# Kernel optimization log

Hardware: AMD Instinct MI355X
Metric: run time of the kernel (lower is better)

The kernel has to match this reference:

```python
import jax, jax.numpy as jnp
import numpy as np

ENTRY_SIZE = 8192
TUPLE_SIZE = 16
N_NEURONS = ENTRY_SIZE // TUPLE_SIZE            # 512
ADDR_SPACE = 2 ** TUPLE_SIZE                     # 65536
BATCH = 4096


def setup_inputs() -> dict:
    key = jax.random.key(0)
    k1, k2, k3 = jax.random.split(key, 3)
    # Binary input bits [B, entry_size]
    inp = jax.random.randint(k1, (BATCH, ENTRY_SIZE), 0, 2, dtype=jnp.int32)
    # Permutation mapping bits -> tuples (identity permutation; arange fill)
    tuple_mapping = jnp.arange(ENTRY_SIZE, dtype=jnp.int64)
    # Dense RAM tables emulating the per-neuron dicts:
    #   counts[n, a] = number of training samples that hit address a in neuron n
    #                  (0 means the address was never trained -> not in dict)
    #   sums[n, a]   = accumulated target sum for that address
    counts = jax.random.randint(k2, (N_NEURONS, ADDR_SPACE), 0, 4, dtype=jnp.int32)
    sums = jax.random.normal(k3, (N_NEURONS, ADDR_SPACE), dtype=jnp.float32)
    return {"input": inp, "tuple_mapping": tuple_mapping, "counts": counts, "sums": sums}


def reference(input, tuple_mapping, counts, sums):
    """RegressionWisard.predict with centrality='mean'.

    input:  [B, entry_size] binary bits (int32)
    tuple_mapping: [entry_size] permutation (int)
    counts: [n_neurons, 2^tuple_size] int32 RAM hit counts
    sums:   [n_neurons, 2^tuple_size] float32 RAM target sums
    """
    B = input.shape[0]
    # Map and group bits into tuples: [B, N, T]
    mapped = jnp.take(input, tuple_mapping, axis=1).reshape(B, N_NEURONS, TUPLE_SIZE)
    # Binary address per (sample, neuron); tidx flips so bit 0 is the MSB.
    pow2 = (jnp.int32(1) << jnp.arange(TUPLE_SIZE - 1, -1, -1, dtype=jnp.int32))
    addr = jnp.einsum("bnt,t->bn", mapped, pow2)  # [B, N], values in [0, 2^T)
    neuron_idx = jnp.arange(N_NEURONS, dtype=jnp.int32)[None, :]  # [1, N]
    c = counts[neuron_idx, addr]  # [B, N]
    s = sums[neuron_idx, addr]    # [B, N]
    trained = c > 0               # dict-membership (torch.isin) equivalent
    response = jnp.sum(jnp.where(trained, s, jnp.float32(0)), axis=1)      # [B]
    counters = jnp.sum(jnp.where(trained, c, 0), axis=1).astype(s.dtype)   # [B]
    return jnp.nan_to_num(response / counters)
```

## Files before the change

kernel.cpp:

```cpp
#include <hip/hip_runtime.h>


typedef float f32x4 __attribute__((ext_vector_type(4)));
typedef int   i32x4 __attribute__((ext_vector_type(4)));

constexpr int BATCH   = 4096;
constexpr int ENTRY   = 8192;
constexpr int TUP     = 16;
constexpr int NEUR    = ENTRY / TUP;
constexpr int SPB_A   = 4;
constexpr int QSPLIT  = 8;
constexpr int QSIZE   = 65536 / QSPLIT;

constexpr size_t ADDR_BYTES = (size_t)NEUR * BATCH * 2;
constexpr size_t ACC_OFF    = ADDR_BYTES;
constexpr size_t WS_NEED    = ADDR_BYTES + (size_t)BATCH * 8;

__global__ __launch_bounds__(256) void zero_acc_kernel(unsigned long long* acc) {
    acc[blockIdx.x * 256 + threadIdx.x] = 0ull;
}

__global__ __launch_bounds__(256) void phaseA_kernel(
    const int* __restrict__ input,
    const int* __restrict__ mapping,
    unsigned short* __restrict__ addr_out)
{
    __shared__ unsigned int packed[SPB_A][ENTRY / 32];
    const int tid  = threadIdx.x;
    const int lane = tid & 63;
    const int wv   = tid >> 6;
    const int b0   = blockIdx.x * SPB_A;
    constexpr int CH = ENTRY / 64;

    for (int i0 = wv * 4; i0 < SPB_A * CH; i0 += 16) {
        int v[4];
        #pragma unroll
        for (int u = 0; u < 4; ++u) {
            const int i = i0 + u, r = i >> 7, c = i & 127;
            v[u] = __builtin_nontemporal_load(
                &input[(size_t)(b0 + r) * ENTRY + c * 64 + lane]);
        }
        #pragma unroll
        for (int u = 0; u < 4; ++u) {
            const int i = i0 + u, r = i >> 7, c = i & 127;
            const unsigned long long m = __ballot(v[u] & 1);
            if (lane == 0) {
                packed[r][c * 2]     = (unsigned int)(m);
                packed[r][c * 2 + 1] = (unsigned int)(m >> 32);
            }
        }
    }
    __syncthreads();

    #pragma unroll
    for (int k = 0; k < 2; ++k) {
        const int n = tid + k * 256;
        const int* map_n = mapping + n * TUP;
        int addr[SPB_A] = {0, 0, 0, 0};
        #pragma unroll
        for (int t = 0; t < TUP; ++t) {
            const int j = map_n[t];
            const unsigned w = j >> 5, sh = j & 31;
            #pragma unroll
            for (int s = 0; s < SPB_A; ++s)
                addr[s] = (addr[s] << 1) | ((packed[s][w] >> sh) & 1);
        }
        uint2 pk;
        pk.x = (unsigned)addr[0] | ((unsigned)addr[1] << 16);
        pk.y = (unsigned)addr[2] | ((unsigned)addr[3] << 16);
        *(uint2*)(addr_out + (size_t)n * BATCH + b0) = pk;
    }
}

__global__ __launch_bounds__(256) void phaseB_kernel(
    const int*   __restrict__ counts,
    const float* __restrict__ sums,
    const unsigned short* __restrict__ addr,
    unsigned long long* __restrict__ acc)
{
    __shared__ float         s_tab[QSIZE];
    __shared__ unsigned char c_tab[QSIZE];
    const int tid = threadIdx.x;
    const int n   = blockIdx.x >> 3;
    const int q   = blockIdx.x & (QSPLIT - 1);
    const size_t base = ((size_t)n << 16) + ((size_t)q * QSIZE);

    const f32x4* s4 = (const f32x4*)(sums + base);
    const i32x4* c4 = (const i32x4*)(counts + base);
    f32x4 vs[8]; i32x4 vc[8];
    #pragma unroll
    for (int i = 0; i < 8; ++i) vs[i] = __builtin_nontemporal_load(&s4[tid + 256 * i]);
    #pragma unroll
    for (int i = 0; i < 8; ++i) vc[i] = __builtin_nontemporal_load(&c4[tid + 256 * i]);
    #pragma unroll
    for (int i = 0; i < 8; ++i) {
        ((f32x4*)s_tab)[tid + 256 * i] = vs[i];
        *(uchar4*)&c_tab[(tid + 256 * i) * 4] =
            make_uchar4((unsigned char)vc[i].x, (unsigned char)vc[i].y,
                        (unsigned char)vc[i].z, (unsigned char)vc[i].w);
    }
    __syncthreads();

    const unsigned short* arow = addr + ((size_t)n << 12);
    #pragma unroll
    for (int i = tid; i < BATCH; i += 256) {
        const int a = arow[i];
        if ((a >> 13) == q) {
            const int local = a & (QSIZE - 1);
            const int c = c_tab[local];
            if (c) {
                const long long r = (long long)__float2int_rn(s_tab[local] * 16777216.0f);
                atomicAdd(&acc[i], (unsigned long long)((r << 20) + (long long)c));
            }
        }
    }
}

__global__ __launch_bounds__(256) void phaseC_kernel(
    const unsigned long long* __restrict__ acc, float* __restrict__ out)
{
    const int i = blockIdx.x * 256 + threadIdx.x;
    const long long v = (long long)acc[i];
    const int cnt = (int)(v & 0xFFFFF);
    const long long rq = v >> 20;
    out[i] = (cnt > 0)
        ? (float)(((double)rq * (1.0 / 16777216.0)) / (double)cnt)
        : 0.0f;
}

__global__ __launch_bounds__(256) void wisard_direct_kernel(
    const int* __restrict__ input, const int* __restrict__ mapping,
    const int* __restrict__ counts, const float* __restrict__ sums,
    float* __restrict__ out)
{
    __shared__ unsigned int packed[ENTRY / 32];
    __shared__ float s_resp[4];
    __shared__ int   s_cnt [4];
    const int tid = threadIdx.x, lane = tid & 63, wv = tid >> 6;
    const int* row = input + (size_t)blockIdx.x * ENTRY;
    for (int i = wv; i < ENTRY / 64; i += 4) {
        const unsigned long long m = __ballot(row[i * 64 + lane] & 1);
        if (lane == 0) {
            packed[i * 2] = (unsigned int)m;
            packed[i * 2 + 1] = (unsigned int)(m >> 32);
        }
    }
    __syncthreads();
    float resp = 0.0f; int cnt = 0;
    #pragma unroll
    for (int k = 0; k < 2; ++k) {
        const int n = tid + k * 256;
        const int* map_n = mapping + n * TUP;
        int a = 0;
        #pragma unroll
        for (int t = 0; t < TUP; ++t) {
            const int j = map_n[t];
            a = (a << 1) | ((packed[j >> 5] >> (j & 31)) & 1);
        }
        const int idx = (n << 16) | a;
        const int c = counts[idx];
        if (c > 0) { resp += sums[idx]; cnt += c; }
    }
    #pragma unroll
    for (int off = 32; off > 0; off >>= 1) {
        resp += __shfl_down(resp, off, 64);
        cnt  += __shfl_down(cnt,  off, 64);
    }
    if (lane == 0) { s_resp[wv] = resp; s_cnt[wv] = cnt; }
    __syncthreads();
    if (tid == 0) {
        float r = s_resp[0] + s_resp[1] + s_resp[2] + s_resp[3];
        int   c = s_cnt[0] + s_cnt[1] + s_cnt[2] + s_cnt[3];
        out[blockIdx.x] = (c > 0) ? (r / (float)c) : 0.0f;
    }
}

extern "C" void kernel_launch(void* const* d_in, const int* in_sizes, int n_in,
                              void* d_out, int out_size, void* d_ws, size_t ws_size,
                              hipStream_t stream) {
    (void)in_sizes; (void)n_in; (void)out_size;
    const int*   input   = (const int*)d_in[0];
    const int*   mapping = (const int*)d_in[1];
    const int*   counts  = (const int*)d_in[2];
    const float* sums    = (const float*)d_in[3];
    float*       out     = (float*)d_out;

    if (ws_size >= WS_NEED) {
        unsigned short*     addr_ws = (unsigned short*)d_ws;
        unsigned long long* acc     = (unsigned long long*)((char*)d_ws + ACC_OFF);
        zero_acc_kernel<<<BATCH / 256, 256, 0, stream>>>(acc);
        phaseA_kernel<<<BATCH / SPB_A, 256, 0, stream>>>(input, mapping, addr_ws);
        phaseB_kernel<<<NEUR * QSPLIT, 256, 0, stream>>>(counts, sums, addr_ws, acc);
        phaseC_kernel<<<BATCH / 256, 256, 0, stream>>>(acc, out);
    } else {
        wisard_direct_kernel<<<BATCH, 256, 0, stream>>>(input, mapping, counts, sums, out);
    }
}
```

Measured before the change: 378.1 us.

## Vectorize bit packing, fold acc zeroing into phase A, split RAM tables finer

Phase A now loads each input row with 128-bit vector loads and packs 32 bits per thread directly, replacing the wave ballot loop. Zeroing of the accumulator moves into phase A, which removes one kernel launch. Phase B splits each neuron's table into 16 quarters instead of 8, giving smaller shared-memory tables and more blocks, which should raise occupancy. Each thread now reads 16 contiguous addresses with vector loads. The cost is that every block re-reads the full address row twice as often, and atomics go to contiguous acc slots per thread.

After: 413.2 us. 9.3% more time.

```diff
diff --git a/kernel.cpp b/kernel.cpp
--- a/kernel.cpp
+++ b/kernel.cpp
@@ -1,54 +1,49 @@
 #include <hip/hip_runtime.h>
 
 
-typedef float f32x4 __attribute__((ext_vector_type(4)));
-typedef int   i32x4 __attribute__((ext_vector_type(4)));
+typedef float          f32x4 __attribute__((ext_vector_type(4)));
+typedef int            i32x4 __attribute__((ext_vector_type(4)));
+typedef unsigned short u16x8 __attribute__((ext_vector_type(8)));
 
 constexpr int BATCH   = 4096;
 constexpr int ENTRY   = 8192;
 constexpr int TUP     = 16;
 constexpr int NEUR    = ENTRY / TUP;
 constexpr int SPB_A   = 4;
-constexpr int QSPLIT  = 8;
+constexpr int QSPLIT  = 16;
 constexpr int QSIZE   = 65536 / QSPLIT;
 
 constexpr size_t ADDR_BYTES = (size_t)NEUR * BATCH * 2;
 constexpr size_t ACC_OFF    = ADDR_BYTES;
 constexpr size_t WS_NEED    = ADDR_BYTES + (size_t)BATCH * 8;
 
-__global__ __launch_bounds__(256) void zero_acc_kernel(unsigned long long* acc) {
-    acc[blockIdx.x * 256 + threadIdx.x] = 0ull;
-}
-
 __global__ __launch_bounds__(256) void phaseA_kernel(
     const int* __restrict__ input,
     const int* __restrict__ mapping,
-    unsigned short* __restrict__ addr_out)
+    unsigned short* __restrict__ addr_out,
+    unsigned long long* __restrict__ acc)
 {
     __shared__ unsigned int packed[SPB_A][ENTRY / 32];
-    const int tid  = threadIdx.x;
-    const int lane = tid & 63;
-    const int wv   = tid >> 6;
-    const int b0   = blockIdx.x * SPB_A;
-    constexpr int CH = ENTRY / 64;
+    const int tid = threadIdx.x;
+    const int b0  = blockIdx.x * SPB_A;
 
-    for (int i0 = wv * 4; i0 < SPB_A * CH; i0 += 16) {
-        int v[4];
+    if (blockIdx.x < BATCH / 256) acc[blockIdx.x * 256 + tid] = 0ull;
+
+    #pragma unroll
+    for (int r = 0; r < SPB_A; ++r) {
+        const i32x4* src = (const i32x4*)(input + (size_t)(b0 + r) * ENTRY) + tid * 8;
+        i32x4 v[8];
         #pragma unroll
-        for (int u = 0; u < 4; ++u) {
-            const int i = i0 + u, r = i >> 7, c = i & 127;
-            v[u] = __builtin_nontemporal_load(
-                &input[(size_t)(b0 + r) * ENTRY + c * 64 + lane]);
+        for (int u = 0; u < 8; ++u) v[u] = __builtin_nontemporal_load(&src[u]);
+        unsigned w = 0;
+        #pragma unroll
+        for (int u = 0; u < 8; ++u) {
+            w |= ((unsigned)v[u].x & 1u) << (u * 4 + 0);
+            w |= ((unsigned)v[u].y & 1u) << (u * 4 + 1);
+            w |= ((unsigned)v[u].z & 1u) << (u * 4 + 2);
+            w |= ((unsigned)v[u].w & 1u) << (u * 4 + 3);
         }
-        #pragma unroll
-        for (int u = 0; u < 4; ++u) {
-            const int i = i0 + u, r = i >> 7, c = i & 127;
-            const unsigned long long m = __ballot(v[u] & 1);
-            if (lane == 0) {
-                packed[r][c * 2]     = (unsigned int)(m);
-                packed[r][c * 2 + 1] = (unsigned int)(m >> 32);
-            }
-        }
+        packed[r][tid] = w;
     }
     __syncthreads();
 
@@ -81,19 +76,19 @@
     __shared__ float         s_tab[QSIZE];
     __shared__ unsigned char c_tab[QSIZE];
     const int tid = threadIdx.x;
-    const int n   = blockIdx.x >> 3;
+    const int n   = blockIdx.x >> 4;
     const int q   = blockIdx.x & (QSPLIT - 1);
-    const size_t base = ((size_t)n << 16) + ((size_t)q * QSIZE);
+    const size_t base = ((size_t)n << 16) + (size_t)q * QSIZE;
 
     const f32x4* s4 = (const f32x4*)(sums + base);
     const i32x4* c4 = (const i32x4*)(counts + base);
-    f32x4 vs[8]; i32x4 vc[8];
+    f32x4 vs[4]; i32x4 vc[4];
     #pragma unroll
-    for (int i = 0; i < 8; ++i) vs[i] = __builtin_nontemporal_load(&s4[tid + 256 * i]);
+    for (int i = 0; i < 4; ++i) vs[i] = __builtin_nontemporal_load(&s4[tid + 256 * i]);
     #pragma unroll
-    for (int i = 0; i < 8; ++i) vc[i] = __builtin_nontemporal_load(&c4[tid + 256 * i]);
+    for (int i = 0; i < 4; ++i) vc[i] = __builtin_nontemporal_load(&c4[tid + 256 * i]);
     #pragma unroll
-    for (int i = 0; i < 8; ++i) {
+    for (int i = 0; i < 4; ++i) {
         ((f32x4*)s_tab)[tid + 256 * i] = vs[i];
         *(uchar4*)&c_tab[(tid + 256 * i) * 4] =
             make_uchar4((unsigned char)vc[i].x, (unsigned char)vc[i].y,
@@ -101,16 +96,20 @@
     }
     __syncthreads();
 
-    const unsigned short* arow = addr + ((size_t)n << 12);
+    const unsigned short* arow = addr + ((size_t)n << 12) + tid * 16;
+    const u16x8 a0 = *(const u16x8*)(arow);
+    const u16x8 a1 = *(const u16x8*)(arow + 8);
     #pragma unroll
-    for (int i = tid; i < BATCH; i += 256) {
-        const int a = arow[i];
-        if ((a >> 13) == q) {
+    for (int j = 0; j < 16; ++j) {
+        const int a = (j < 8) ? a0[j] : a1[j - 8];
+        if ((a >> 12) == q) {
             const int local = a & (QSIZE - 1);
             const int c = c_tab[local];
             if (c) {
-                const long long r = (long long)__float2int_rn(s_tab[local] * 16777216.0f);
-                atomicAdd(&acc[i], (unsigned long long)((r << 20) + (long long)c));
+                const long long r =
+                    (long long)__float2int_rn(s_tab[local] * 16777216.0f);
+                atomicAdd(&acc[tid * 16 + j],
+                          (unsigned long long)((r << 20) + (long long)c));
             }
         }
     }
@@ -188,8 +187,7 @@
     if (ws_size >= WS_NEED) {
         unsigned short*     addr_ws = (unsigned short*)d_ws;
         unsigned long long* acc     = (unsigned long long*)((char*)d_ws + ACC_OFF);
-        zero_acc_kernel<<<BATCH / 256, 256, 0, stream>>>(acc);
-        phaseA_kernel<<<BATCH / SPB_A, 256, 0, stream>>>(input, mapping, addr_ws);
+        phaseA_kernel<<<BATCH / SPB_A, 256, 0, stream>>>(input, mapping, addr_ws, acc);
         phaseB_kernel<<<NEUR * QSPLIT, 256, 0, stream>>>(counts, sums, addr_ws, acc);
         phaseC_kernel<<<BATCH / 256, 256, 0, stream>>>(acc, out);
     } else {
```
